# Kernel optimization log

Measured on AMD Instinct MI355X. Metric: run time of the kernel, lower is better.

The kernel has to match this reference:

```python
import jax, jax.numpy as jnp
import numpy as np

NUM_ATTN = 4
D = 128          # embed_dim (query_dims['t1'] == key_dims['t1'])
NPATH = 8        # num_query_path
BATCH = 65536
LN_EPS = 1e-6


def _layernorm(x, g, b):
    # normalize over last axis (torch-style LayerNorm on [batch, d])
    mu = jnp.mean(x, axis=-1, keepdims=True)
    var = jnp.mean((x - mu) ** 2, axis=-1, keepdims=True)
    return g * (x - mu) / jnp.sqrt(var + LN_EPS) + b


def setup_inputs() -> dict:
    key = jax.random.key(0)
    ks = jax.random.split(key, 8)
    xav_attn = float(np.sqrt(6.0 / (2 * D + NUM_ATTN)))
    xav_w = float(np.sqrt(6.0 / (D + D)))
    xav_b = float(np.sqrt(6.0 / (D + 1)))
    return {
        "query_embed": jax.random.normal(ks[0], (1, D, BATCH), jnp.float32),
        "key_embeds": jax.random.normal(ks[1], (NPATH, D, BATCH), jnp.float32),
        "atten_vecs": jax.random.uniform(ks[2], (2 * D, NUM_ATTN), jnp.float32, -xav_attn, xav_attn),
        "ln_g": jnp.ones((D,), jnp.float32),
        "ln_b": jnp.zeros((D,), jnp.float32),
        "post_W": jax.random.uniform(ks[3], (D, D), jnp.float32, -xav_w, xav_w),
        "post_B": jax.random.uniform(ks[4], (D, 1), jnp.float32, -xav_b, xav_b),
        "post_ln_g": jnp.ones((D,), jnp.float32),
        "post_ln_b": jnp.zeros((D,), jnp.float32),
    }


def reference(query_embed, key_embeds, atten_vecs, ln_g, ln_b, post_W, post_B, post_ln_g, post_ln_b):
    # query_embed: [1, d, b]; key_embeds: [n, d, b]
    q = jnp.broadcast_to(query_embed[0], key_embeds.shape)          # [n, d, b]
    concat = jnp.concatenate([q, key_embeds], axis=1).transpose(0, 2, 1)  # [n, b, 2d]
    attn = jnp.einsum('nbd,dk->nbk', concat, atten_vecs)            # [n, b, k]
    attn = jax.nn.softmax(jax.nn.leaky_relu(attn, 0.01), axis=0)    # softmax over query paths
    attn = attn.transpose(1, 2, 0)                                  # [b, k, n]
    keys = key_embeds.transpose(2, 0, 1)                            # [b, n, d]
    combined = jnp.einsum('bkn,bnd->bkd', attn, keys)               # [b, k, d]
    combined = jnp.sum(combined, axis=1) * (1.0 / NUM_ATTN)         # [b, d]
    combined = jax.nn.relu(combined).T                              # [d, b]
    # layernorm branch
    combined = combined + query_embed[0]                            # [d, b]
    combined = _layernorm(combined.T, ln_g, ln_b).T                 # [d, b]
    # post matmul branch
    linear = post_W @ combined + post_B                             # [d, b]
    linear = linear + combined
    linear = _layernorm(linear.T, post_ln_g, post_ln_b).T           # [d, b]
    return linear
```

## Files before the change

### kernel.cpp

```cpp
#include <hip/hip_runtime.h>

#define DD 128
#define NP 8
#define NK 4
#define NB 65536
#define COLS 64
#define PSTR 37
#define CST 136

typedef __bf16 bf16x8 __attribute__((ext_vector_type(8)));
typedef float  f32x4  __attribute__((ext_vector_type(4)));

__global__ __launch_bounds__(256) void k1_attn_combine(
    const float* __restrict__ q, const float* __restrict__ keys,
    const float* __restrict__ A, float* __restrict__ y,
    float* __restrict__ mu_o, float* __restrict__ rs_o)
{
    __shared__ float lds[4 * COLS * PSTR];
    const int col = threadIdx.x & 63;
    const int dg  = __builtin_amdgcn_readfirstlane(threadIdx.x >> 6);
    const int b   = blockIdx.x * COLS + col;
    const int dbase = dg * 32;

    float qd[NK] = {0.f, 0.f, 0.f, 0.f};
    float kd[NP][NK];
    #pragma unroll
    for (int n = 0; n < NP; ++n)
        #pragma unroll
        for (int k = 0; k < NK; ++k) kd[n][k] = 0.f;

    #pragma unroll 4
    for (int dd = 0; dd < 32; ++dd) {
        const int d = dbase + dd;
        const float4 at = *(const float4*)(A + d * NK);
        const float4 ab = *(const float4*)(A + (DD + d) * NK);
        const float qv = q[d * NB + b];
        qd[0] += qv * at.x; qd[1] += qv * at.y;
        qd[2] += qv * at.z; qd[3] += qv * at.w;
        #pragma unroll
        for (int n = 0; n < NP; ++n) {
            const float kv = keys[(n * DD + d) * NB + b];
            kd[n][0] += kv * ab.x; kd[n][1] += kv * ab.y;
            kd[n][2] += kv * ab.z; kd[n][3] += kv * ab.w;
        }
    }

    {
        float* my = &lds[(dg * COLS + col) * PSTR];
        #pragma unroll
        for (int k = 0; k < NK; ++k) my[k] = qd[k];
        #pragma unroll
        for (int n = 0; n < NP; ++n)
            #pragma unroll
            for (int k = 0; k < NK; ++k) my[4 + n * NK + k] = kd[n][k];
    }
    __syncthreads();
    #pragma unroll
    for (int ii = 0; ii < 9; ++ii) {
        const int i = dg * 9 + ii;
        float s = lds[(0 * COLS + col) * PSTR + i]
                + lds[(1 * COLS + col) * PSTR + i]
                + lds[(2 * COLS + col) * PSTR + i]
                + lds[(3 * COLS + col) * PSTR + i];
        lds[col * PSTR + i] = s;
    }
    __syncthreads();

    float z[NP][NK];
    {
        float qs[NK];
        #pragma unroll
        for (int k = 0; k < NK; ++k) qs[k] = lds[col * PSTR + k];
        float mx[NK] = {-3.4e38f, -3.4e38f, -3.4e38f, -3.4e38f};
        #pragma unroll
        for (int n = 0; n < NP; ++n)
            #pragma unroll
            for (int k = 0; k < NK; ++k) {
                float v = qs[k] + lds[col * PSTR + 4 + n * NK + k];
                v = (v >= 0.f) ? v : 0.01f * v;
                z[n][k] = v;
                mx[k] = fmaxf(mx[k], v);
            }
        float S[NK] = {0.f, 0.f, 0.f, 0.f};
        #pragma unroll
        for (int n = 0; n < NP; ++n)
            #pragma unroll
            for (int k = 0; k < NK; ++k) {
                const float e = __expf(z[n][k] - mx[k]);
                z[n][k] = e;
                S[k] += e;
            }
        #pragma unroll
        for (int k = 0; k < NK; ++k) S[k] = 1.f / S[k];
        #pragma unroll
        for (int n = 0; n < NP; ++n)
            z[n][0] = 0.25f * (z[n][0] * S[0] + z[n][1] * S[1] +
                               z[n][2] * S[2] + z[n][3] * S[3]);
    }
    float w[NP];
    #pragma unroll
    for (int n = 0; n < NP; ++n) w[n] = z[n][0];
    __syncthreads();

    float sum = 0.f, ssq = 0.f;
    #pragma unroll 4
    for (int dd = 0; dd < 32; ++dd) {
        const int d = dbase + dd;
        float acc = 0.f;
        #pragma unroll
        for (int n = 0; n < NP; ++n) acc += w[n] * keys[(n * DD + d) * NB + b];
        const float yv = fmaxf(acc, 0.f) + q[d * NB + b];
        y[d * NB + b] = yv;
        sum += yv;
        ssq += yv * yv;
    }
    lds[(dg * COLS + col) * PSTR + 0] = sum;
    lds[(dg * COLS + col) * PSTR + 1] = ssq;
    __syncthreads();
    if (dg == 0) {
        float ts = 0.f, tq = 0.f;
        #pragma unroll
        for (int g = 0; g < 4; ++g) {
            ts += lds[(g * COLS + col) * PSTR + 0];
            tq += lds[(g * COLS + col) * PSTR + 1];
        }
        const float mu  = ts * (1.f / DD);
        const float var = tq * (1.f / DD) - mu * mu;
        mu_o[b] = mu;
        rs_o[b] = rsqrtf(var + 1e-6f);
    }
}

__global__ __launch_bounds__(256, 3) void k2_mfma(
    const float* y, const float* __restrict__ mu_a, const float* __restrict__ rs_a,
    const float* __restrict__ g1, const float* __restrict__ b1,
    const float* __restrict__ W,  const float* __restrict__ Bv,
    const float* __restrict__ g2, const float* __restrict__ b2,
    float* out)
{
    __shared__ __align__(16) __bf16 c_l[COLS * CST];
    __shared__ float sums2[4][COLS][2];

    const int t    = threadIdx.x;
    const int col  = t & 63;
    const int qtr  = t >> 6;
    const int gcol0 = blockIdx.x * COLS;
    const int b    = gcol0 + col;
    const float mu = mu_a[b], rs = rs_a[b];

    {
        bf16x8 cb[4];
        #pragma unroll
        for (int j = 0; j < 4; ++j)
            #pragma unroll
            for (int e = 0; e < 8; ++e) {
                const int d = qtr * 32 + j * 8 + e;
                cb[j][e] = (__bf16)(g1[d] * ((y[d * NB + b] - mu) * rs) + b1[d]);
            }
        #pragma unroll
        for (int j = 0; j < 4; ++j)
            *(bf16x8*)(c_l + col * CST + qtr * 32 + j * 8) = cb[j];
    }
    __syncthreads();

    const int lane = t & 63;
    const int c16  = lane & 15;
    const int dg   = lane >> 4;

    bf16x8 wf[2][4];
    #pragma unroll
    for (int mi = 0; mi < 2; ++mi)
        #pragma unroll
        for (int kk = 0; kk < 4; ++kk) {
            const int row = qtr * 32 + mi * 16 + c16;
            const int kb  = kk * 32 + dg * 8;
            const float4 wa = *(const float4*)(W + row * DD + kb);
            const float4 wb = *(const float4*)(W + row * DD + kb + 4);
            bf16x8 f;
            f[0] = (__bf16)wa.x; f[1] = (__bf16)wa.y;
            f[2] = (__bf16)wa.z; f[3] = (__bf16)wa.w;
            f[4] = (__bf16)wb.x; f[5] = (__bf16)wb.y;
            f[6] = (__bf16)wb.z; f[7] = (__bf16)wb.w;
            wf[mi][kk] = f;
        }

    f32x4 acc[2][4];
    #pragma unroll
    for (int mi = 0; mi < 2; ++mi)
        #pragma unroll
        for (int nf = 0; nf < 4; ++nf)
            acc[mi][nf] = (f32x4){0.f, 0.f, 0.f, 0.f};

    #pragma unroll
    for (int kk = 0; kk < 4; ++kk) {
        bf16x8 bfv[4];
        #pragma unroll
        for (int nf = 0; nf < 4; ++nf)
            bfv[nf] = *(const bf16x8*)(c_l + (nf * 16 + c16) * CST + kk * 32 + dg * 8);
        #pragma unroll
        for (int mi = 0; mi < 2; ++mi)
            #pragma unroll
            for (int nf = 0; nf < 4; ++nf)
                acc[mi][nf] = __builtin_amdgcn_mfma_f32_16x16x32_bf16(
                    wf[mi][kk], bfv[nf], acc[mi][nf], 0, 0, 0);
    }

    float Brow[2][4], grow[2][4], brow[2][4];
    #pragma unroll
    for (int mi = 0; mi < 2; ++mi)
        #pragma unroll
        for (int r = 0; r < 4; ++r) {
            const int row = qtr * 32 + mi * 16 + dg * 4 + r;
            Brow[mi][r] = Bv[row];
            grow[mi][r] = g2[row];
            brow[mi][r] = b2[row];
        }

    float vv[2][4][4];
    float ps[4] = {0.f,0.f,0.f,0.f}, pq[4] = {0.f,0.f,0.f,0.f};
    #pragma unroll
    for (int nf = 0; nf < 4; ++nf) {
        const int cl = nf * 16 + c16;
        #pragma unroll
        for (int mi = 0; mi < 2; ++mi)
            #pragma unroll
            for (int r = 0; r < 4; ++r) {
                const int row = qtr * 32 + mi * 16 + dg * 4 + r;
                const float cres = (float)c_l[cl * CST + row];
                const float v = acc[mi][nf][r] + Brow[mi][r] + cres;
                vv[mi][nf][r] = v;
                ps[nf] += v;
                pq[nf] += v * v;
            }
    }
    #pragma unroll
    for (int nf = 0; nf < 4; ++nf) {
        ps[nf] += __shfl_xor(ps[nf], 16); ps[nf] += __shfl_xor(ps[nf], 32);
        pq[nf] += __shfl_xor(pq[nf], 16); pq[nf] += __shfl_xor(pq[nf], 32);
    }
    if (dg == 0) {
        #pragma unroll
        for (int nf = 0; nf < 4; ++nf) {
            sums2[qtr][nf * 16 + c16][0] = ps[nf];
            sums2[qtr][nf * 16 + c16][1] = pq[nf];
        }
    }
    __syncthreads();

    #pragma unroll
    for (int nf = 0; nf < 4; ++nf) {
        const int cl = nf * 16 + c16;
        float ts = 0.f, tq = 0.f;
        #pragma unroll
        for (int g = 0; g < 4; ++g) {
            ts += sums2[g][cl][0];
            tq += sums2[g][cl][1];
        }
        const float mu2 = ts * (1.f / DD);
        const float rs2 = rsqrtf(tq * (1.f / DD) - mu2 * mu2 + 1e-6f);
        #pragma unroll
        for (int mi = 0; mi < 2; ++mi)
            #pragma unroll
            for (int r = 0; r < 4; ++r) {
                const int row = qtr * 32 + mi * 16 + dg * 4 + r;
                out[row * NB + gcol0 + cl] =
                    grow[mi][r] * ((vv[mi][nf][r] - mu2) * rs2) + brow[mi][r];
            }
    }
}

extern "C" void kernel_launch(void* const* d_in, const int* in_sizes, int n_in,
                              void* d_out, int out_size, void* d_ws, size_t ws_size,
                              hipStream_t stream)
{
    const float* q    = (const float*)d_in[0];
    const float* keys = (const float*)d_in[1];
    const float* A    = (const float*)d_in[2];
    const float* g1   = (const float*)d_in[3];
    const float* b1   = (const float*)d_in[4];
    const float* W    = (const float*)d_in[5];
    const float* Bv   = (const float*)d_in[6];
    const float* g2   = (const float*)d_in[7];
    const float* b2   = (const float*)d_in[8];
    float* out = (float*)d_out;

    float* mu = (float*)d_ws;
    float* rs = mu + NB;

    k1_attn_combine<<<NB / COLS, 256, 0, stream>>>(q, keys, A, out, mu, rs);
    k2_mfma<<<NB / COLS, 256, 0, stream>>>(out, mu, rs, g1, b1, W, Bv, g2, b2, out);
}
```

Baseline: 121.8 us.

## Fuse attention-combine and MFMA post-matmul kernels into one kernel

Merges the two kernels into a single kernel. The intermediate y stays in registers and the first layernorm statistics are reduced in LDS, instead of y being written to global memory, stored as per-column mu/rs, and read back by the second kernel. This removes a full 32 MB write and read round trip of the intermediate plus one launch. In exchange, register pressure rises because 32 y values are held per thread, and the launch bound is raised to 4 waves, which risks spills or lower occupancy.

```diff
diff --git a/kernel.cpp b/kernel.cpp
--- a/kernel.cpp
+++ b/kernel.cpp
@@ -11,15 +11,24 @@
 typedef __bf16 bf16x8 __attribute__((ext_vector_type(8)));
 typedef float  f32x4  __attribute__((ext_vector_type(4)));
 
-__global__ __launch_bounds__(256) void k1_attn_combine(
+__global__ __launch_bounds__(256, 4) void fused_all(
     const float* __restrict__ q, const float* __restrict__ keys,
-    const float* __restrict__ A, float* __restrict__ y,
-    float* __restrict__ mu_o, float* __restrict__ rs_o)
+    const float* __restrict__ A,
+    const float* __restrict__ g1, const float* __restrict__ b1,
+    const float* __restrict__ W,  const float* __restrict__ Bv,
+    const float* __restrict__ g2, const float* __restrict__ b2,
+    float* __restrict__ out)
 {
-    __shared__ float lds[4 * COLS * PSTR];
-    const int col = threadIdx.x & 63;
-    const int dg  = __builtin_amdgcn_readfirstlane(threadIdx.x >> 6);
-    const int b   = blockIdx.x * COLS + col;
+    __shared__ __align__(16) float lds[4 * COLS * PSTR];
+    __bf16* c_l        = (__bf16*)lds;
+    float (*sred)[COLS][2]  = (float (*)[COLS][2])((char*)lds + 18432);
+    float (*sums2)[COLS][2] = (float (*)[COLS][2])((char*)lds + 20480);
+
+    const int t   = threadIdx.x;
+    const int col = t & 63;
+    const int dg  = __builtin_amdgcn_readfirstlane(t >> 6);
+    const int gcol0 = blockIdx.x * COLS;
+    const int b   = gcol0 + col;
     const int dbase = dg * 32;
 
     float qd[NK] = {0.f, 0.f, 0.f, 0.f};
@@ -66,8 +75,9 @@
     }
     __syncthreads();
 
-    float z[NP][NK];
+    float w[NP];
     {
+        float z[NP][NK];
         float qs[NK];
         #pragma unroll
         for (int k = 0; k < NK; ++k) qs[k] = lds[col * PSTR + k];
@@ -94,14 +104,11 @@
         for (int k = 0; k < NK; ++k) S[k] = 1.f / S[k];
         #pragma unroll
         for (int n = 0; n < NP; ++n)
-            z[n][0] = 0.25f * (z[n][0] * S[0] + z[n][1] * S[1] +
-                               z[n][2] * S[2] + z[n][3] * S[3]);
-    }
-    float w[NP];
-    #pragma unroll
-    for (int n = 0; n < NP; ++n) w[n] = z[n][0];
-    __syncthreads();
-
+            w[n] = 0.25f * (z[n][0] * S[0] + z[n][1] * S[1] +
+                            z[n][2] * S[2] + z[n][3] * S[3]);
+    }
+
+    float y[32];
     float sum = 0.f, ssq = 0.f;
     #pragma unroll 4
     for (int dd = 0; dd < 32; ++dd) {
@@ -110,43 +117,22 @@
         #pragma unroll
         for (int n = 0; n < NP; ++n) acc += w[n] * keys[(n * DD + d) * NB + b];
         const float yv = fmaxf(acc, 0.f) + q[d * NB + b];
-        y[d * NB + b] = yv;
+        y[dd] = yv;
         sum += yv;
         ssq += yv * yv;
     }
-    lds[(dg * COLS + col) * PSTR + 0] = sum;
-    lds[(dg * COLS + col) * PSTR + 1] = ssq;
-    __syncthreads();
-    if (dg == 0) {
-        float ts = 0.f, tq = 0.f;
-        #pragma unroll
-        for (int g = 0; g < 4; ++g) {
-            ts += lds[(g * COLS + col) * PSTR + 0];
-            tq += lds[(g * COLS + col) * PSTR + 1];
-        }
-        const float mu  = ts * (1.f / DD);
-        const float var = tq * (1.f / DD) - mu * mu;
-        mu_o[b] = mu;
-        rs_o[b] = rsqrtf(var + 1e-6f);
-    }
-}
-
-__global__ __launch_bounds__(256, 3) void k2_mfma(
-    const float* y, const float* __restrict__ mu_a, const float* __restrict__ rs_a,
-    const float* __restrict__ g1, const float* __restrict__ b1,
-    const float* __restrict__ W,  const float* __restrict__ Bv,
-    const float* __restrict__ g2, const float* __restrict__ b2,
-    float* out)
-{
-    __shared__ __align__(16) __bf16 c_l[COLS * CST];
-    __shared__ float sums2[4][COLS][2];
-
-    const int t    = threadIdx.x;
-    const int col  = t & 63;
-    const int qtr  = t >> 6;
-    const int gcol0 = blockIdx.x * COLS;
-    const int b    = gcol0 + col;
-    const float mu = mu_a[b], rs = rs_a[b];
+    __syncthreads();
+    sred[dg][col][0] = sum;
+    sred[dg][col][1] = ssq;
+    __syncthreads();
+    float ts1 = 0.f, tq1 = 0.f;
+    #pragma unroll
+    for (int g = 0; g < 4; ++g) {
+        ts1 += sred[g][col][0];
+        tq1 += sred[g][col][1];
+    }
+    const float mu = ts1 * (1.f / DD);
+    const float rs = rsqrtf(tq1 * (1.f / DD) - mu * mu + 1e-6f);
 
     {
         bf16x8 cb[4];
@@ -154,26 +140,26 @@
         for (int j = 0; j < 4; ++j)
             #pragma unroll
             for (int e = 0; e < 8; ++e) {
-                const int d = qtr * 32 + j * 8 + e;
-                cb[j][e] = (__bf16)(g1[d] * ((y[d * NB + b] - mu) * rs) + b1[d]);
+                const int d = dbase + j * 8 + e;
+                cb[j][e] = (__bf16)(g1[d] * ((y[j * 8 + e] - mu) * rs) + b1[d]);
             }
         #pragma unroll
         for (int j = 0; j < 4; ++j)
-            *(bf16x8*)(c_l + col * CST + qtr * 32 + j * 8) = cb[j];
+            *(bf16x8*)(c_l + col * CST + dbase + j * 8) = cb[j];
     }
     __syncthreads();
 
     const int lane = t & 63;
     const int c16  = lane & 15;
-    const int dg   = lane >> 4;
+    const int dg4  = lane >> 4;
 
     bf16x8 wf[2][4];
     #pragma unroll
     for (int mi = 0; mi < 2; ++mi)
         #pragma unroll
         for (int kk = 0; kk < 4; ++kk) {
-            const int row = qtr * 32 + mi * 16 + c16;
-            const int kb  = kk * 32 + dg * 8;
+            const int row = dg * 32 + mi * 16 + c16;
+            const int kb  = kk * 32 + dg4 * 8;
             const float4 wa = *(const float4*)(W + row * DD + kb);
             const float4 wb = *(const float4*)(W + row * DD + kb + 4);
             bf16x8 f;
@@ -196,7 +182,7 @@
         bf16x8 bfv[4];
         #pragma unroll
         for (int nf = 0; nf < 4; ++nf)
-            bfv[nf] = *(const bf16x8*)(c_l + (nf * 16 + c16) * CST + kk * 32 + dg * 8);
+            bfv[nf] = *(const bf16x8*)(c_l + (nf * 16 + c16) * CST + kk * 32 + dg4 * 8);
         #pragma unroll
         for (int mi = 0; mi < 2; ++mi)
             #pragma unroll
@@ -210,7 +196,7 @@
     for (int mi = 0; mi < 2; ++mi)
         #pragma unroll
         for (int r = 0; r < 4; ++r) {
-            const int row = qtr * 32 + mi * 16 + dg * 4 + r;
+            const int row = dg * 32 + mi * 16 + dg4 * 4 + r;
             Brow[mi][r] = Bv[row];
             grow[mi][r] = g2[row];
             brow[mi][r] = b2[row];
@@ -225,7 +211,7 @@
         for (int mi = 0; mi < 2; ++mi)
             #pragma unroll
             for (int r = 0; r < 4; ++r) {
-                const int row = qtr * 32 + mi * 16 + dg * 4 + r;
+                const int row = dg * 32 + mi * 16 + dg4 * 4 + r;
                 const float cres = (float)c_l[cl * CST + row];
                 const float v = acc[mi][nf][r] + Brow[mi][r] + cres;
                 vv[mi][nf][r] = v;
@@ -238,11 +224,11 @@
         ps[nf] += __shfl_xor(ps[nf], 16); ps[nf] += __shfl_xor(ps[nf], 32);
         pq[nf] += __shfl_xor(pq[nf], 16); pq[nf] += __shfl_xor(pq[nf], 32);
     }
-    if (dg == 0) {
+    if (dg4 == 0) {
         #pragma unroll
         for (int nf = 0; nf < 4; ++nf) {
-            sums2[qtr][nf * 16 + c16][0] = ps[nf];
-            sums2[qtr][nf * 16 + c16][1] = pq[nf];
+            sums2[dg][nf * 16 + c16][0] = ps[nf];
+            sums2[dg][nf * 16 + c16][1] = pq[nf];
         }
     }
     __syncthreads();
@@ -262,7 +248,7 @@
         for (int mi = 0; mi < 2; ++mi)
             #pragma unroll
             for (int r = 0; r < 4; ++r) {
-                const int row = qtr * 32 + mi * 16 + dg * 4 + r;
+                const int row = dg * 32 + mi * 16 + dg4 * 4 + r;
                 out[row * NB + gcol0 + cl] =
                     grow[mi][r] * ((vv[mi][nf][r] - mu2) * rs2) + brow[mi][r];
             }
@@ -284,9 +270,5 @@
     const float* b2   = (const float*)d_in[8];
     float* out = (float*)d_out;
 
-    float* mu = (float*)d_ws;
-    float* rs = mu + NB;
-
-    k1_attn_combine<<<NB / COLS, 256, 0, stream>>>(q, keys, A, out, mu, rs);
-    k2_mfma<<<NB / COLS, 256, 0, stream>>>(out, mu, rs, g1, b1, W, Bv, g2, b2, out);
+    fused_all<<<NB / COLS, 256, 0, stream>>>(q, keys, A, g1, b1, W, Bv, g2, b2, out);
 }
```

New measurement: 114.8 us. 5.7% less time.
